# Optimization experiments

Hardware: AMD Instinct MI355X
Metric: run time of the kernel (lower is better)

## Reference

```python
import jax, jax.numpy as jnp
import numpy as np

# Kernel codes matching style 'L;O2;P2;Y2,1,1;R0.5;W1,1'
KERNEL_CODES = ['L', 'O', 'P', 'Y', 'R', 'W']
SM_TEMP = 1.0


def _norm_sq(q, k):
    # q: [n,l,h,e], k: [n,s,h,e] -> [n,h,l,s]
    q2 = jnp.einsum('nlhe,nlhe->nhl', q, q)[..., None]        # [n,h,l,1]
    k2 = jnp.einsum('nshe,nshe->nhs', k, k)[:, :, None, :]     # [n,h,1,s]
    qk = jnp.einsum('nlhe,nshe->nhls', q, k)
    return q2 + k2 - 2.0 * qk


def _kernel(code, q, k):
    if code == 'L':
        return jnp.einsum('nlhe,nshe->nhls', q, k)
    if code == 'O':  # -log(1 + ns^(p/2)), p=2
        return -jnp.log1p(_norm_sq(q, k))
    if code == 'P':  # -(ns)^(p/2), p=2
        return -_norm_sq(q, k)
    if code == 'Y':  # (alpha*<q,k> + c)^p, p=2, alpha=1, c=1
        d = jnp.einsum('nlhe,nshe->nhls', q, k)
        return (d + 1.0) ** 2
    if code == 'R':  # exp(-gamma*ns), gamma=0.5
        return jnp.exp(-0.5 * _norm_sq(q, k))
    if code == 'W':  # cos(ns/a)*exp(-ns/b), a=b=1
        ns = _norm_sq(q, k)
        return jnp.cos(ns) * jnp.exp(-ns)
    raise ValueError(code)


def setup_inputs() -> dict:
    key = jax.random.key(0)
    k1, k2, k3, k4 = jax.random.split(key, 4)
    N, L, S, H, E, K = 2, 1024, 1024, 8, 64, 6
    return {
        'query': jax.random.normal(k1, (N, L, H, E), dtype=jnp.float32),
        'key': jax.random.normal(k2, (N, S, H, E), dtype=jnp.float32),
        'attn_mask_add': jnp.zeros((N, L, S), dtype=jnp.float32),
        'key_lengths_add': jnp.zeros((N, S), dtype=jnp.float32),
        'M': jax.random.uniform(k3, (H, E, K), dtype=jnp.float32),
        'C': jax.random.uniform(k4, (K, H, E, E), dtype=jnp.float32),
    }


def reference(query, key, attn_mask_add, key_lengths_add, M, C):
    # mixture weights pi: [n,l,h,k]
    pi = jax.nn.softmax(jnp.einsum('nlhe,hek->nlhk', query, M), axis=-1)
    out = None
    for c, code in enumerate(KERNEL_CODES):
        # htilde = tanh(query @ C[c]): [n,l,h,e]
        htilde = jnp.tanh(jnp.einsum('nlhe,hef->nlhf', query, C[c]))
        qk = _kernel(code, htilde, key)                    # [n,h,l,s]
        qk = qk + attn_mask_add[:, None] + key_lengths_add[:, None, None, :]
        sm = jax.nn.softmax(SM_TEMP * qk, axis=-1)
        w = jnp.transpose(pi[..., c], (0, 2, 1))[..., None]  # [n,h,l,1]
        term = sm * w
        out = term if out is None else out + term
    return out
```

## Files before the change

### kernel.cpp

```cpp
#include <hip/hip_runtime.h>
#include <hip/hip_bf16.h>
#include <math.h>

#define N_  2
#define H_  8
#define G_  16
#define L_  1024
#define S_  1024
#define E_  64
#define NC_ 6

typedef __attribute__((ext_vector_type(4))) float floatx4;
typedef __attribute__((ext_vector_type(8))) short short8;

#define MFMA16 __builtin_amdgcn_mfma_f32_16x16x32_bf16

#define AHAT_OFF   0
#define AHAT_BYTES (NC_*G_*L_*128*2)
#define KHAT_OFF   (AHAT_OFF + AHAT_BYTES)
#define KHAT_BYTES (G_*S_*128*2)
#define PI_OFF     (KHAT_OFF + KHAT_BYTES)
#define PI_BYTES   (NC_*G_*L_*4)
#define HSQ_OFF    (PI_OFF + PI_BYTES)
#define HSQ_BYTES  (NC_*G_*L_*4)
#define KSQ_OFF    (HSQ_OFF + HSQ_BYTES)
#define KSQ_BYTES  (G_*S_*4)

__device__ __forceinline__ float ftanh(float x) {
  return 1.0f - 2.0f * __builtin_amdgcn_rcpf(__expf(2.0f*x) + 1.0f);
}

__global__ __launch_bounds__(256) void k_htilde(
    const float* __restrict__ q, const float* __restrict__ C,
    __hip_bfloat16* __restrict__ Ahat, float* __restrict__ hsq) {
  extern __shared__ char smraw[];
  float* qs = (float*)smraw;
  float* Cs = qs + 128*68;

  const int lch = blockIdx.x, c = blockIdx.y, g = blockIdx.z;
  const int n = g >> 3, h = g & 7;
  const int l0 = lch * 128;
  const int t = threadIdx.x;

  for (int u = t; u < 2048; u += 256) {
    int row = u >> 4, seg = u & 15;
    *(float4*)(qs + row*68 + seg*4) =
      *(const float4*)(q + (((size_t)(n*L_ + l0 + row))*H_ + h)*E_ + seg*4);
  }
  for (int u = t; u < 1024; u += 256) {
    int e = u >> 4, seg = u & 15;
    *(float4*)(Cs + e*68 + seg*4) =
      *(const float4*)(C + (((size_t)(c*8 + h))*64 + e)*64 + seg*4);
  }
  __syncthreads();

  const int rg = t >> 3, fg = t & 7;
  float acc[4][8];
  #pragma unroll
  for (int i = 0; i < 4; i++)
    #pragma unroll
    for (int j = 0; j < 8; j++) acc[i][j] = 0.0f;

  #pragma unroll 4
  for (int e0 = 0; e0 < 64; e0 += 4) {
    float4 q4[4];
    #pragma unroll
    for (int i = 0; i < 4; i++)
      q4[i] = *(const float4*)(qs + (rg*4 + i)*68 + e0);
    #pragma unroll
    for (int ee = 0; ee < 4; ee++) {
      float4 ca = *(const float4*)(Cs + (e0+ee)*68 + fg*8);
      float4 cb = *(const float4*)(Cs + (e0+ee)*68 + fg*8 + 4);
      float c8[8] = {ca.x, ca.y, ca.z, ca.w, cb.x, cb.y, cb.z, cb.w};
      #pragma unroll
      for (int i = 0; i < 4; i++) {
        float qv = (ee == 0) ? q4[i].x : (ee == 1) ? q4[i].y
                 : (ee == 2) ? q4[i].z : q4[i].w;
        #pragma unroll
        for (int j = 0; j < 8; j++) acc[i][j] = fmaf(qv, c8[j], acc[i][j]);
      }
    }
  }

  #pragma unroll
  for (int i = 0; i < 4; i++) {
    int l = l0 + rg*4 + i;
    size_t rowb = (((size_t)(c*G_ + g))*L_ + l) * 128;
    float ss = 0.0f;
    short8 hi8, lo8;
    #pragma unroll
    for (int j = 0; j < 8; j++) {
      float hv = ftanh(acc[i][j]);
      ss += hv*hv;
      __hip_bfloat16 hi = __float2bfloat16(hv);
      __hip_bfloat16 lo = __float2bfloat16(hv - __bfloat162float(hi));
      short hs, ls;
      __builtin_memcpy(&hs, &hi, 2);
      __builtin_memcpy(&ls, &lo, 2);
      hi8[j] = hs; lo8[j] = ls;
    }
    *(short8*)((char*)Ahat + (rowb + fg*8)*2)      = hi8;
    *(short8*)((char*)Ahat + (rowb + 64 + fg*8)*2) = lo8;
    ss += __shfl_xor(ss, 1); ss += __shfl_xor(ss, 2); ss += __shfl_xor(ss, 4);
    if (fg == 0) hsq[((size_t)(c*G_ + g))*L_ + l] = ss;
  }
}

__global__ __launch_bounds__(256) void k_pi(
    const float* __restrict__ q, const float* __restrict__ M,
    float* __restrict__ pi_t) {
  __shared__ float Ms[384];
  const int g = blockIdx.x >> 2, lch = blockIdx.x & 3;
  const int n = g >> 3, h = g & 7;
  const int t = threadIdx.x;
  const int l = lch*256 + t;
  for (int u = t; u < 384; u += 256) Ms[u] = M[h*384 + u];
  __syncthreads();
  const float* qrow = q + (((size_t)(n*L_ + l))*H_ + h)*E_;
  float p[6] = {0.f, 0.f, 0.f, 0.f, 0.f, 0.f};
  #pragma unroll 8
  for (int e = 0; e < 64; e++) {
    float qv = qrow[e];
    #pragma unroll
    for (int k = 0; k < 6; k++) p[k] = fmaf(qv, Ms[e*6 + k], p[k]);
  }
  float mx = p[0];
  #pragma unroll
  for (int k = 1; k < 6; k++) mx = fmaxf(mx, p[k]);
  float den = 0.f;
  #pragma unroll
  for (int k = 0; k < 6; k++) den += __expf(p[k] - mx);
  float rden = __builtin_amdgcn_rcpf(den);
  #pragma unroll
  for (int k = 0; k < 6; k++)
    pi_t[((size_t)(k*G_ + g))*L_ + l] = __expf(p[k] - mx) * rden;
}

__global__ __launch_bounds__(256) void k_key(
    const float* __restrict__ key, __hip_bfloat16* __restrict__ Khat,
    float* __restrict__ ksq) {
  int t = threadIdx.x; int wv = t >> 6; int lane = t & 63;
  int r = blockIdx.x*4 + wv;
  int g = r >> 10; int s = r & 1023; int n = g >> 3; int h = g & 7;
  float v = key[(((size_t)(n*S_ + s))*H_ + h)*E_ + lane];
  __hip_bfloat16 hi = __float2bfloat16(v);
  __hip_bfloat16 lo = __float2bfloat16(v - __bfloat162float(hi));
  size_t base = ((size_t)g*S_ + s)*128;
  Khat[base + lane]      = hi;
  Khat[base + 64 + lane] = lo;
  float sq = v*v;
  #pragma unroll
  for (int off = 32; off; off >>= 1) sq += __shfl_xor(sq, off);
  if (lane == 0) ksq[(size_t)g*S_ + s] = sq;
}

#define LDS_A6LO  0
#define LDS_ZRED  13824
#define LDS_MRED  15360
#define LDS_CST   16896
#define LDS_TOTAL 17664

__global__ __launch_bounds__(256, 2) void k_main(
    const __hip_bfloat16* __restrict__ Ahat, const __hip_bfloat16* __restrict__ Khat,
    const float* __restrict__ hsq, const float* __restrict__ ksq,
    const float* __restrict__ mask, const float* __restrict__ klen,
    const float* __restrict__ pi_t, float* __restrict__ out) {
  extern __shared__ char smraw[];
  char*   A6     = smraw + LDS_A6LO;
  float*  zred   = (float*)(smraw + LDS_ZRED);
  float*  mred   = (float*)(smraw + LDS_MRED);
  float2* cst    = (float2*)(smraw + LDS_CST);

  const int l0 = blockIdx.x * 16; const int g = blockIdx.y; const int n = g >> 3;
  const int t = threadIdx.x; const int w = t >> 6; const int lane = t & 63;
  const int quad = lane >> 4; const int lc = lane & 15;

  #pragma unroll
  for (int rep = 0; rep < 3; rep++) {
    int u = t + rep*256; int row = u >> 3, seg = u & 7;
    int cc = row >> 4, lr = row & 15;
    *(int4*)(A6 + row*144 + seg*16) =
      *(const int4*)((const char*)Ahat +
          (((size_t)(cc*G_ + g))*L_ + l0 + lr)*256 + 128 + seg*16);
  }

  short8 ah[6][2];
  #pragma unroll
  for (int cc = 0; cc < 6; cc++) {
    const char* arow = (const char*)Ahat + (((size_t)(cc*G_ + g))*L_ + l0 + lc)*256;
    ah[cc][0] = *(const short8*)(arow + quad*16);
    ah[cc][1] = *(const short8*)(arow + 64 + quad*16);
  }

  float h1p = 1.0f  + hsq[((size_t)(1*G_ + g))*L_ + l0 + lc];
  float nh2 = 64.0f - hsq[((size_t)(2*G_ + g))*L_ + l0 + lc];
  float h4h = -0.5f * hsq[((size_t)(4*G_ + g))*L_ + l0 + lc];
  float nh5 = -hsq[((size_t)(5*G_ + g))*L_ + l0 + lc];

  __syncthreads();

  auto LOADK = [&](int st, short8 (&bf)[4]) {
    const char* base = (const char*)Khat +
        (((size_t)g)*S_ + st*64 + w*16 + lc)*256 + quad*16;
    #pragma unroll
    for (int kt = 0; kt < 4; kt++)
      bf[kt] = *(const short8*)(base + kt*64);
  };

  float Zc0 = 0.f, Zc1 = 0.f, Zc2 = 0.f, Zc3 = 0.f, zp = 0.f;
  float m3 = -INFINITY, z3 = 0.f;

  auto SWEEP1 = [&](int st, const short8 (&bf)[4]) {
    int sb = st*64 + w*16 + quad*4;
    float4 mk4 = *(const float4*)(mask + ((size_t)(n*L_ + l0 + lc))*S_ + sb);
    float4 kl4 = *(const float4*)(klen + (size_t)n*S_ + sb);
    float4 kq4 = *(const float4*)(ksq  + (size_t)g*S_ + sb);
    float kq[4] = {kq4.x, kq4.y, kq4.z, kq4.w};
    float mv[4], Ev[4];
    mv[0] = mk4.x + kl4.x; mv[1] = mk4.y + kl4.y;
    mv[2] = mk4.z + kl4.z; mv[3] = mk4.w + kl4.w;
    #pragma unroll
    for (int i = 0; i < 4; i++) Ev[i] = __expf(mv[i]);
    #pragma unroll
    for (int c = 0; c < 6; c++) {
      short8 al0 = *(const short8*)(A6 + (c*16 + lc)*144 + quad*16);
      short8 al1 = *(const short8*)(A6 + (c*16 + lc)*144 + 64 + quad*16);
      floatx4 a = {0.f, 0.f, 0.f, 0.f};
      a = MFMA16(bf[0], ah[c][0], a, 0,0,0);
      a = MFMA16(bf[1], ah[c][1], a, 0,0,0);
      a = MFMA16(bf[0], al0,      a, 0,0,0);
      a = MFMA16(bf[1], al1,      a, 0,0,0);
      a = MFMA16(bf[2], ah[c][0], a, 0,0,0);
      a = MFMA16(bf[3], ah[c][1], a, 0,0,0);
      #pragma unroll
      for (int i = 0; i < 4; i++) {
        float d = a[i];
        if (c == 0) {
          Zc0 = fmaf(Ev[i], __expf(d), Zc0);
        } else if (c == 1) {
          Zc1 = fmaf(Ev[i], __builtin_amdgcn_rcpf(fmaf(-2.f, d, h1p + kq[i])), Zc1);
        } else if (c == 2) {
          zp += __expf(fmaf(2.f, d, nh2 - kq[i] + mv[i]));
        } else if (c == 3) {
          float tt = d + 1.f;
          float x  = fmaf(tt, tt, mv[i]);
          float mn = fmaxf(m3, x);
          float e  = __expf(fminf(m3, x) - mn);
          z3 = (x > m3) ? fmaf(z3, e, 1.0f) : (z3 + e);
          m3 = mn;
        } else if (c == 4) {
          Zc2 = fmaf(Ev[i], __expf(__expf(d + fmaf(-0.5f, kq[i], h4h))), Zc2);
        } else {
          float a5 = fmaf(2.f, d, nh5 - kq[i]);
          Zc3 = fmaf(Ev[i], __expf(__cosf(a5) * __expf(a5)), Zc3);
        }
      }
    }
  };

  {
    short8 bA[4], bB[4];
    LOADK(0, bA);
    #pragma unroll 1
    for (int st = 0; st < 16; st += 2) {
      LOADK(st + 1, bB);
      SWEEP1(st, bA);
      LOADK((st + 2) & 15, bA);
      SWEEP1(st + 1, bB);
    }
  }

  #pragma unroll
  for (int off = 16; off < 64; off <<= 1) {
    Zc0 += __shfl_xor(Zc0, off); Zc1 += __shfl_xor(Zc1, off);
    Zc2 += __shfl_xor(Zc2, off); Zc3 += __shfl_xor(Zc3, off);
    zp  += __shfl_xor(zp,  off);
    float mo = __shfl_xor(m3, off);
    float zo = __shfl_xor(z3, off);
    float mn = fmaxf(m3, mo);
    float e  = __expf(fminf(m3, mo) - mn);
    z3 = (mo > m3) ? fmaf(z3, e, zo) : fmaf(zo, e, z3);
    m3 = mn;
  }
  if (lane < 16) {
    zred[w*96 + 0*16 + lc] = Zc0; mred[w*96 + 0*16 + lc] = 0.f;
    zred[w*96 + 1*16 + lc] = Zc1; mred[w*96 + 1*16 + lc] = 0.f;
    zred[w*96 + 2*16 + lc] = zp;  mred[w*96 + 2*16 + lc] = 0.f;
    zred[w*96 + 3*16 + lc] = z3;  mred[w*96 + 3*16 + lc] = m3;
    zred[w*96 + 4*16 + lc] = Zc2; mred[w*96 + 4*16 + lc] = 0.f;
    zred[w*96 + 5*16 + lc] = Zc3; mred[w*96 + 5*16 + lc] = 0.f;
  }
  __syncthreads();
  if (t < 96) {
    int c = t >> 4;
    float z = zred[t], m = mred[t];
    if (c == 3) {
      #pragma unroll
      for (int w2 = 1; w2 < 4; w2++) {
        float mo = mred[w2*96 + t], zo = zred[w2*96 + t];
        float mn = fmaxf(m, mo);
        float e  = __expf(fminf(m, mo) - mn);
        z = (mo > m) ? fmaf(z, e, zo) : fmaf(zo, e, z);
        m = mn;
      }
    } else {
      #pragma unroll
      for (int w2 = 1; w2 < 4; w2++) z += zred[w2*96 + t];
    }
    float piv = pi_t[((size_t)((t >> 4)*G_ + g))*L_ + l0 + (t & 15)];
    cst[t] = make_float2(piv / z, m);
  }
  __syncthreads();

  float ac0 = cst[0*16 + lc].x, ac1 = cst[1*16 + lc].x, ac2 = cst[2*16 + lc].x;
  float ac3 = cst[3*16 + lc].x, ac4 = cst[4*16 + lc].x, ac5 = cst[5*16 + lc].x;
  float m3f = cst[3*16 + lc].y;

  auto SWEEP2 = [&](int st, const short8 (&bf)[4]) {
    int sb = st*64 + w*16 + quad*4;
    float4 mk4 = *(const float4*)(mask + ((size_t)(n*L_ + l0 + lc))*S_ + sb);
    float4 kl4 = *(const float4*)(klen + (size_t)n*S_ + sb);
    float4 kq4 = *(const float4*)(ksq  + (size_t)g*S_ + sb);
    float kq[4] = {kq4.x, kq4.y, kq4.z, kq4.w};
    float mv[4], Ev[4];
    mv[0] = mk4.x + kl4.x; mv[1] = mk4.y + kl4.y;
    mv[2] = mk4.z + kl4.z; mv[3] = mk4.w + kl4.w;
    #pragma unroll
    for (int i = 0; i < 4; i++) Ev[i] = __expf(mv[i]);
    float Sacc[4] = {0.f, 0.f, 0.f, 0.f};
    float Gg[4]   = {0.f, 0.f, 0.f, 0.f};
    #pragma unroll
    for (int c = 0; c < 6; c++) {
      short8 al0 = *(const short8*)(A6 + (c*16 + lc)*144 + quad*16);
      short8 al1 = *(const short8*)(A6 + (c*16 + lc)*144 + 64 + quad*16);
      floatx4 a = {0.f, 0.f, 0.f, 0.f};
      a = MFMA16(bf[0], ah[c][0], a, 0,0,0);
      a = MFMA16(bf[1], ah[c][1], a, 0,0,0);
      a = MFMA16(bf[0], al0,      a, 0,0,0);
      a = MFMA16(bf[1], al1,      a, 0,0,0);
      a = MFMA16(bf[2], ah[c][0], a, 0,0,0);
      a = MFMA16(bf[3], ah[c][1], a, 0,0,0);
      #pragma unroll
      for (int i = 0; i < 4; i++) {
        float d = a[i];
        if (c == 0) {
          Sacc[i] = fmaf(ac0, __expf(d), Sacc[i]);
        } else if (c == 1) {
          Sacc[i] = fmaf(ac1, __builtin_amdgcn_rcpf(fmaf(-2.f, d, h1p + kq[i])), Sacc[i]);
        } else if (c == 2) {
          Gg[i] = fmaf(ac2, __expf(fmaf(2.f, d, nh2 - kq[i] + mv[i])), Gg[i]);
        } else if (c == 3) {
          float tt = d + 1.f;
          float x  = fmaf(tt, tt, mv[i]);
          Gg[i] = fmaf(ac3, __expf(x - m3f), Gg[i]);
        } else if (c == 4) {
          Sacc[i] = fmaf(ac4, __expf(__expf(d + fmaf(-0.5f, kq[i], h4h))), Sacc[i]);
        } else {
          float a5 = fmaf(2.f, d, nh5 - kq[i]);
          Sacc[i] = fmaf(ac5, __expf(__cosf(a5) * __expf(a5)), Sacc[i]);
        }
      }
    }
    float4 ov;
    ov.x = fmaf(Ev[0], Sacc[0], Gg[0]);
    ov.y = fmaf(Ev[1], Sacc[1], Gg[1]);
    ov.z = fmaf(Ev[2], Sacc[2], Gg[2]);
    ov.w = fmaf(Ev[3], Sacc[3], Gg[3]);
    *(float4*)(out + (((size_t)g)*L_ + l0 + lc)*S_ + sb) = ov;
  };

  {
    short8 bA[4], bB[4];
    LOADK(0, bA);
    #pragma unroll 1
    for (int st = 0; st < 16; st += 2) {
      LOADK(st + 1, bB);
      SWEEP2(st, bA);
      LOADK((st + 2) & 15, bA);
      SWEEP2(st + 1, bB);
    }
  }
}

extern "C" void kernel_launch(void* const* d_in, const int* in_sizes, int n_in,
                              void* d_out, int out_size, void* d_ws, size_t ws_size,
                              hipStream_t stream) {
  (void)in_sizes; (void)n_in; (void)out_size; (void)ws_size;
  const float* q    = (const float*)d_in[0];
  const float* key  = (const float*)d_in[1];
  const float* mask = (const float*)d_in[2];
  const float* klen = (const float*)d_in[3];
  const float* M    = (const float*)d_in[4];
  const float* C    = (const float*)d_in[5];
  char* ws = (char*)d_ws;
  __hip_bfloat16* Ahat = (__hip_bfloat16*)(ws + AHAT_OFF);
  __hip_bfloat16* Khat = (__hip_bfloat16*)(ws + KHAT_OFF);
  float* pi_t    = (float*)(ws + PI_OFF);
  float* hsq     = (float*)(ws + HSQ_OFF);
  float* ksq     = (float*)(ws + KSQ_OFF);
  float* out = (float*)d_out;

  k_htilde<<<dim3(8, 6, 16), 256, 52224, stream>>>(q, C, Ahat, hsq);
  k_key<<<4096, 256, 0, stream>>>(key, Khat, ksq);
  k_pi<<<64, 256, 0, stream>>>(q, M, pi_t);
  k_main<<<dim3(64, 16), 256, LDS_TOTAL, stream>>>(Ahat, Khat, hsq, ksq, mask, klen,
                                                   pi_t, out);
}
```

Measured before the change: 202.7 us.

## Merge prep kernels, precombine mask and key lengths, restructure main loop

The three preprocessing kernels become one launch that dispatches on block index, and a new branch writes the sum of mask and key-length bias into an extra workspace buffer. The main kernel reads that single buffer instead of two arrays. It moves the hi parts of A for components 4 and 5 into LDS to cut register use. Both sweeps now issue all six MFMA groups before the transcendental math, with single-buffered prefetch of K and mask/ksq, and the mask is folded into the exponent arguments. In exchange, the combined mask buffer costs an extra 8MB write and read pass per call, and the A rows for components 4 and 5 are now read from LDS.

```diff
diff --git a/kernel.cpp b/kernel.cpp
--- a/kernel.cpp
+++ b/kernel.cpp
@@ -25,151 +25,170 @@
 #define HSQ_BYTES  (NC_*G_*L_*4)
 #define KSQ_OFF    (HSQ_OFF + HSQ_BYTES)
 #define KSQ_BYTES  (G_*S_*4)
+#define MKL_OFF    (KSQ_OFF + KSQ_BYTES)
+#define MKL_BYTES  (N_*L_*S_*4)
 
 __device__ __forceinline__ float ftanh(float x) {
   return 1.0f - 2.0f * __builtin_amdgcn_rcpf(__expf(2.0f*x) + 1.0f);
 }
 
-__global__ __launch_bounds__(256) void k_htilde(
+__global__ __launch_bounds__(256) void k_prep(
     const float* __restrict__ q, const float* __restrict__ C,
-    __hip_bfloat16* __restrict__ Ahat, float* __restrict__ hsq) {
+    const float* __restrict__ key, const float* __restrict__ M,
+    const float* __restrict__ mask, const float* __restrict__ klen,
+    __hip_bfloat16* __restrict__ Ahat, float* __restrict__ hsq,
+    __hip_bfloat16* __restrict__ Khat, float* __restrict__ ksq,
+    float* __restrict__ pi_t, float* __restrict__ mkl) {
   extern __shared__ char smraw[];
-  float* qs = (float*)smraw;
-  float* Cs = qs + 128*68;
-
-  const int lch = blockIdx.x, c = blockIdx.y, g = blockIdx.z;
-  const int n = g >> 3, h = g & 7;
-  const int l0 = lch * 128;
+  const int bx = blockIdx.x;
   const int t = threadIdx.x;
 
-  for (int u = t; u < 2048; u += 256) {
-    int row = u >> 4, seg = u & 15;
-    *(float4*)(qs + row*68 + seg*4) =
-      *(const float4*)(q + (((size_t)(n*L_ + l0 + row))*H_ + h)*E_ + seg*4);
-  }
-  for (int u = t; u < 1024; u += 256) {
-    int e = u >> 4, seg = u & 15;
-    *(float4*)(Cs + e*68 + seg*4) =
-      *(const float4*)(C + (((size_t)(c*8 + h))*64 + e)*64 + seg*4);
-  }
-  __syncthreads();
-
-  const int rg = t >> 3, fg = t & 7;
-  float acc[4][8];
-  #pragma unroll
-  for (int i = 0; i < 4; i++)
-    #pragma unroll
-    for (int j = 0; j < 8; j++) acc[i][j] = 0.0f;
-
-  #pragma unroll 4
-  for (int e0 = 0; e0 < 64; e0 += 4) {
-    float4 q4[4];
+  if (bx < 768) {
+    float* qs = (float*)smraw;
+    float* Cs = qs + 128*68;
+    const int g = bx / 48, r6 = bx % 48, c = r6 >> 3, lch = r6 & 7;
+    const int n = g >> 3, h = g & 7;
+    const int l0 = lch * 128;
+
+    for (int u = t; u < 2048; u += 256) {
+      int row = u >> 4, seg = u & 15;
+      *(float4*)(qs + row*68 + seg*4) =
+        *(const float4*)(q + (((size_t)(n*L_ + l0 + row))*H_ + h)*E_ + seg*4);
+    }
+    for (int u = t; u < 1024; u += 256) {
+      int e = u >> 4, seg = u & 15;
+      *(float4*)(Cs + e*68 + seg*4) =
+        *(const float4*)(C + (((size_t)(c*8 + h))*64 + e)*64 + seg*4);
+    }
+    __syncthreads();
+
+    const int rg = t >> 3, fg = t & 7;
+    float acc[4][8];
     #pragma unroll
     for (int i = 0; i < 4; i++)
-      q4[i] = *(const float4*)(qs + (rg*4 + i)*68 + e0);
-    #pragma unroll
-    for (int ee = 0; ee < 4; ee++) {
-      float4 ca = *(const float4*)(Cs + (e0+ee)*68 + fg*8);
-      float4 cb = *(const float4*)(Cs + (e0+ee)*68 + fg*8 + 4);
-      float c8[8] = {ca.x, ca.y, ca.z, ca.w, cb.x, cb.y, cb.z, cb.w};
-      #pragma unroll
-      for (int i = 0; i < 4; i++) {
-        float qv = (ee == 0) ? q4[i].x : (ee == 1) ? q4[i].y
-                 : (ee == 2) ? q4[i].z : q4[i].w;
+      #pragma unroll
+      for (int j = 0; j < 8; j++) acc[i][j] = 0.0f;
+
+    #pragma unroll 4
+    for (int e0 = 0; e0 < 64; e0 += 4) {
+      float4 q4[4];
+      #pragma unroll
+      for (int i = 0; i < 4; i++)
+        q4[i] = *(const float4*)(qs + (rg*4 + i)*68 + e0);
+      #pragma unroll
+      for (int ee = 0; ee < 4; ee++) {
+        float4 ca = *(const float4*)(Cs + (e0+ee)*68 + fg*8);
+        float4 cb = *(const float4*)(Cs + (e0+ee)*68 + fg*8 + 4);
+        float c8[8] = {ca.x, ca.y, ca.z, ca.w, cb.x, cb.y, cb.z, cb.w};
         #pragma unroll
-        for (int j = 0; j < 8; j++) acc[i][j] = fmaf(qv, c8[j], acc[i][j]);
-      }
-    }
-  }
-
-  #pragma unroll
-  for (int i = 0; i < 4; i++) {
-    int l = l0 + rg*4 + i;
-    size_t rowb = (((size_t)(c*G_ + g))*L_ + l) * 128;
-    float ss = 0.0f;
-    short8 hi8, lo8;
-    #pragma unroll
-    for (int j = 0; j < 8; j++) {
-      float hv = ftanh(acc[i][j]);
-      ss += hv*hv;
-      __hip_bfloat16 hi = __float2bfloat16(hv);
-      __hip_bfloat16 lo = __float2bfloat16(hv - __bfloat162float(hi));
-      short hs, ls;
-      __builtin_memcpy(&hs, &hi, 2);
-      __builtin_memcpy(&ls, &lo, 2);
-      hi8[j] = hs; lo8[j] = ls;
-    }
-    *(short8*)((char*)Ahat + (rowb + fg*8)*2)      = hi8;
-    *(short8*)((char*)Ahat + (rowb + 64 + fg*8)*2) = lo8;
-    ss += __shfl_xor(ss, 1); ss += __shfl_xor(ss, 2); ss += __shfl_xor(ss, 4);
-    if (fg == 0) hsq[((size_t)(c*G_ + g))*L_ + l] = ss;
+        for (int i = 0; i < 4; i++) {
+          float qv = (ee == 0) ? q4[i].x : (ee == 1) ? q4[i].y
+                   : (ee == 2) ? q4[i].z : q4[i].w;
+          #pragma unroll
+          for (int j = 0; j < 8; j++) acc[i][j] = fmaf(qv, c8[j], acc[i][j]);
+        }
+      }
+    }
+
+    #pragma unroll
+    for (int i = 0; i < 4; i++) {
+      int l = l0 + rg*4 + i;
+      size_t rowb = (((size_t)(c*G_ + g))*L_ + l) * 128;
+      float ss = 0.0f;
+      short8 hi8, lo8;
+      #pragma unroll
+      for (int j = 0; j < 8; j++) {
+        float hv = ftanh(acc[i][j]);
+        ss += hv*hv;
+        __hip_bfloat16 hi = __float2bfloat16(hv);
+        __hip_bfloat16 lo = __float2bfloat16(hv - __bfloat162float(hi));
+        short hs, ls;
+        __builtin_memcpy(&hs, &hi, 2);
+        __builtin_memcpy(&ls, &lo, 2);
+        hi8[j] = hs; lo8[j] = ls;
+      }
+      *(short8*)((char*)Ahat + (rowb + fg*8)*2)      = hi8;
+      *(short8*)((char*)Ahat + (rowb + 64 + fg*8)*2) = lo8;
+      ss += __shfl_xor(ss, 1); ss += __shfl_xor(ss, 2); ss += __shfl_xor(ss, 4);
+      if (fg == 0) hsq[((size_t)(c*G_ + g))*L_ + l] = ss;
+    }
+  } else if (bx < 1024) {
+    const int kb = bx - 768;
+    const int wv = t >> 6, lane = t & 63;
+    #pragma unroll 1
+    for (int it = 0; it < 16; it++) {
+      int r = kb*64 + it*4 + wv;
+      int g = r >> 10, s = r & 1023, n = g >> 3, h = g & 7;
+      float v = key[(((size_t)(n*S_ + s))*H_ + h)*E_ + lane];
+      __hip_bfloat16 hi = __float2bfloat16(v);
+      __hip_bfloat16 lo = __float2bfloat16(v - __bfloat162float(hi));
+      size_t base = ((size_t)g*S_ + s)*128;
+      Khat[base + lane]      = hi;
+      Khat[base + 64 + lane] = lo;
+      float sq = v*v;
+      #pragma unroll
+      for (int off = 32; off; off >>= 1) sq += __shfl_xor(sq, off);
+      if (lane == 0) ksq[(size_t)g*S_ + s] = sq;
+    }
+  } else if (bx < 1088) {
+    float* Ms = (float*)smraw;
+    const int pb = bx - 1024;
+    const int g = pb >> 2, lch = pb & 3;
+    const int n = g >> 3, h = g & 7;
+    const int l = lch*256 + t;
+    for (int u = t; u < 384; u += 256) Ms[u] = M[h*384 + u];
+    __syncthreads();
+    const float* qrow = q + (((size_t)(n*L_ + l))*H_ + h)*E_;
+    float p[6] = {0.f, 0.f, 0.f, 0.f, 0.f, 0.f};
+    #pragma unroll 8
+    for (int e = 0; e < 64; e++) {
+      float qv = qrow[e];
+      #pragma unroll
+      for (int k = 0; k < 6; k++) p[k] = fmaf(qv, Ms[e*6 + k], p[k]);
+    }
+    float mx = p[0];
+    #pragma unroll
+    for (int k = 1; k < 6; k++) mx = fmaxf(mx, p[k]);
+    float den = 0.f;
+    #pragma unroll
+    for (int k = 0; k < 6; k++) den += __expf(p[k] - mx);
+    float rden = __builtin_amdgcn_rcpf(den);
+    #pragma unroll
+    for (int k = 0; k < 6; k++)
+      pi_t[((size_t)(k*G_ + g))*L_ + l] = __expf(p[k] - mx) * rden;
+  } else {
+    const int mb = bx - 1088;
+    const float4* m4 = (const float4*)mask;
+    const float4* k4 = (const float4*)klen;
+    float4* o4 = (float4*)mkl;
+    #pragma unroll 1
+    for (int u = mb*256 + t; u < N_*L_*S_/4; u += 128*256) {
+      int n  = u >> 18;
+      int s4 = u & 255;
+      float4 a = m4[u], b = k4[n*256 + s4];
+      o4[u] = make_float4(a.x+b.x, a.y+b.y, a.z+b.z, a.w+b.w);
+    }
   }
 }
 
-__global__ __launch_bounds__(256) void k_pi(
-    const float* __restrict__ q, const float* __restrict__ M,
-    float* __restrict__ pi_t) {
-  __shared__ float Ms[384];
-  const int g = blockIdx.x >> 2, lch = blockIdx.x & 3;
-  const int n = g >> 3, h = g & 7;
-  const int t = threadIdx.x;
-  const int l = lch*256 + t;
-  for (int u = t; u < 384; u += 256) Ms[u] = M[h*384 + u];
-  __syncthreads();
-  const float* qrow = q + (((size_t)(n*L_ + l))*H_ + h)*E_;
-  float p[6] = {0.f, 0.f, 0.f, 0.f, 0.f, 0.f};
-  #pragma unroll 8
-  for (int e = 0; e < 64; e++) {
-    float qv = qrow[e];
-    #pragma unroll
-    for (int k = 0; k < 6; k++) p[k] = fmaf(qv, Ms[e*6 + k], p[k]);
-  }
-  float mx = p[0];
-  #pragma unroll
-  for (int k = 1; k < 6; k++) mx = fmaxf(mx, p[k]);
-  float den = 0.f;
-  #pragma unroll
-  for (int k = 0; k < 6; k++) den += __expf(p[k] - mx);
-  float rden = __builtin_amdgcn_rcpf(den);
-  #pragma unroll
-  for (int k = 0; k < 6; k++)
-    pi_t[((size_t)(k*G_ + g))*L_ + l] = __expf(p[k] - mx) * rden;
-}
-
-__global__ __launch_bounds__(256) void k_key(
-    const float* __restrict__ key, __hip_bfloat16* __restrict__ Khat,
-    float* __restrict__ ksq) {
-  int t = threadIdx.x; int wv = t >> 6; int lane = t & 63;
-  int r = blockIdx.x*4 + wv;
-  int g = r >> 10; int s = r & 1023; int n = g >> 3; int h = g & 7;
-  float v = key[(((size_t)(n*S_ + s))*H_ + h)*E_ + lane];
-  __hip_bfloat16 hi = __float2bfloat16(v);
-  __hip_bfloat16 lo = __float2bfloat16(v - __bfloat162float(hi));
-  size_t base = ((size_t)g*S_ + s)*128;
-  Khat[base + lane]      = hi;
-  Khat[base + 64 + lane] = lo;
-  float sq = v*v;
-  #pragma unroll
-  for (int off = 32; off; off >>= 1) sq += __shfl_xor(sq, off);
-  if (lane == 0) ksq[(size_t)g*S_ + s] = sq;
-}
-
 #define LDS_A6LO  0
-#define LDS_ZRED  13824
-#define LDS_MRED  15360
-#define LDS_CST   16896
-#define LDS_TOTAL 17664
+#define LDS_A45HI 13824
+#define LDS_ZRED  18432
+#define LDS_MRED  19968
+#define LDS_CST   21504
+#define LDS_TOTAL 22272
 
 __global__ __launch_bounds__(256, 2) void k_main(
     const __hip_bfloat16* __restrict__ Ahat, const __hip_bfloat16* __restrict__ Khat,
     const float* __restrict__ hsq, const float* __restrict__ ksq,
-    const float* __restrict__ mask, const float* __restrict__ klen,
-    const float* __restrict__ pi_t, float* __restrict__ out) {
+    const float* __restrict__ mkl, const float* __restrict__ pi_t,
+    float* __restrict__ out) {
   extern __shared__ char smraw[];
-  char*   A6     = smraw + LDS_A6LO;
-  float*  zred   = (float*)(smraw + LDS_ZRED);
-  float*  mred   = (float*)(smraw + LDS_MRED);
-  float2* cst    = (float2*)(smraw + LDS_CST);
+  char*   A6   = smraw + LDS_A6LO;
+  char*   A45  = smraw + LDS_A45HI;
+  float*  zred = (float*)(smraw + LDS_ZRED);
+  float*  mred = (float*)(smraw + LDS_MRED);
+  float2* cst  = (float2*)(smraw + LDS_CST);
 
   const int l0 = blockIdx.x * 16; const int g = blockIdx.y; const int n = g >> 3;
   const int t = threadIdx.x; const int w = t >> 6; const int lane = t & 63;
@@ -183,10 +202,17 @@
       *(const int4*)((const char*)Ahat +
           (((size_t)(cc*G_ + g))*L_ + l0 + lr)*256 + 128 + seg*16);
   }
-
-  short8 ah[6][2];
+  {
+    int row = t >> 3, seg = t & 7;
+    int cc = 4 + (row >> 4), lr = row & 15;
+    *(int4*)(A45 + row*144 + seg*16) =
+      *(const int4*)((const char*)Ahat +
+          (((size_t)(cc*G_ + g))*L_ + l0 + lr)*256 + seg*16);
+  }
+
+  short8 ah[4][2];
   #pragma unroll
-  for (int cc = 0; cc < 6; cc++) {
+  for (int cc = 0; cc < 4; cc++) {
     const char* arow = (const char*)Ahat + (((size_t)(cc*G_ + g))*L_ + l0 + lc)*256;
     ah[cc][0] = *(const short8*)(arow + quad*16);
     ah[cc][1] = *(const short8*)(arow + 64 + quad*16);
@@ -206,67 +232,63 @@
     for (int kt = 0; kt < 4; kt++)
       bf[kt] = *(const short8*)(base + kt*64);
   };
-
-  float Zc0 = 0.f, Zc1 = 0.f, Zc2 = 0.f, Zc3 = 0.f, zp = 0.f;
-  float m3 = -INFINITY, z3 = 0.f;
-
-  auto SWEEP1 = [&](int st, const short8 (&bf)[4]) {
+  auto LOADS = [&](int st, float4& mk4, float4& kq4) {
     int sb = st*64 + w*16 + quad*4;
-    float4 mk4 = *(const float4*)(mask + ((size_t)(n*L_ + l0 + lc))*S_ + sb);
-    float4 kl4 = *(const float4*)(klen + (size_t)n*S_ + sb);
-    float4 kq4 = *(const float4*)(ksq  + (size_t)g*S_ + sb);
-    float kq[4] = {kq4.x, kq4.y, kq4.z, kq4.w};
-    float mv[4], Ev[4];
-    mv[0] = mk4.x + kl4.x; mv[1] = mk4.y + kl4.y;
-    mv[2] = mk4.z + kl4.z; mv[3] = mk4.w + kl4.w;
-    #pragma unroll
-    for (int i = 0; i < 4; i++) Ev[i] = __expf(mv[i]);
+    mk4 = *(const float4*)(mkl + ((size_t)(n*L_ + l0 + lc))*S_ + sb);
+    kq4 = *(const float4*)(ksq + (size_t)g*S_ + sb);
+  };
+  auto MFMAPH = [&](const short8 (&bf)[4], floatx4 (&acc)[6]) {
     #pragma unroll
     for (int c = 0; c < 6; c++) {
+      short8 h0, h1;
+      if (c < 4) { h0 = ah[c][0]; h1 = ah[c][1]; }
+      else {
+        h0 = *(const short8*)(A45 + ((c-4)*16 + lc)*144 + quad*16);
+        h1 = *(const short8*)(A45 + ((c-4)*16 + lc)*144 + 64 + quad*16);
+      }
       short8 al0 = *(const short8*)(A6 + (c*16 + lc)*144 + quad*16);
       short8 al1 = *(const short8*)(A6 + (c*16 + lc)*144 + 64 + quad*16);
       floatx4 a = {0.f, 0.f, 0.f, 0.f};
-      a = MFMA16(bf[0], ah[c][0], a, 0,0,0);
-      a = MFMA16(bf[1], ah[c][1], a, 0,0,0);
-      a = MFMA16(bf[0], al0,      a, 0,0,0);
-      a = MFMA16(bf[1], al1,      a, 0,0,0);
-      a = MFMA16(bf[2], ah[c][0], a, 0,0,0);
-      a = MFMA16(bf[3], ah[c][1], a, 0,0,0);
+      a = MFMA16(bf[0], h0,  a, 0,0,0);
+      a = MFMA16(bf[1], h1,  a, 0,0,0);
+      a = MFMA16(bf[0], al0, a, 0,0,0);
+      a = MFMA16(bf[1], al1, a, 0,0,0);
+      a = MFMA16(bf[2], h0,  a, 0,0,0);
+      a = MFMA16(bf[3], h1,  a, 0,0,0);
+      acc[c] = a;
+    }
+  };
+
+  float Zc0 = 0.f, Zc1 = 0.f, Zc2 = 0.f, Zc3 = 0.f, zp = 0.f;
+  float m3 = -INFINITY, z3 = 0.f;
+
+  {
+    short8 bf[4]; float4 mk4, kq4;
+    LOADK(0, bf); LOADS(0, mk4, kq4);
+    #pragma unroll 1
+    for (int st = 0; st < 16; st++) {
+      floatx4 acc[6];
+      MFMAPH(bf, acc);
+      LOADK((st + 1) & 15, bf);
+      float mvv[4] = {mk4.x, mk4.y, mk4.z, mk4.w};
+      float kq[4]  = {kq4.x, kq4.y, kq4.z, kq4.w};
       #pragma unroll
       for (int i = 0; i < 4; i++) {
-        float d = a[i];
-        if (c == 0) {
-          Zc0 = fmaf(Ev[i], __expf(d), Zc0);
-        } else if (c == 1) {
-          Zc1 = fmaf(Ev[i], __builtin_amdgcn_rcpf(fmaf(-2.f, d, h1p + kq[i])), Zc1);
-        } else if (c == 2) {
-          zp += __expf(fmaf(2.f, d, nh2 - kq[i] + mv[i]));
-        } else if (c == 3) {
-          float tt = d + 1.f;
-          float x  = fmaf(tt, tt, mv[i]);
-          float mn = fmaxf(m3, x);
-          float e  = __expf(fminf(m3, x) - mn);
-          z3 = (x > m3) ? fmaf(z3, e, 1.0f) : (z3 + e);
-          m3 = mn;
-        } else if (c == 4) {
-          Zc2 = fmaf(Ev[i], __expf(__expf(d + fmaf(-0.5f, kq[i], h4h))), Zc2);
-        } else {
-          float a5 = fmaf(2.f, d, nh5 - kq[i]);
-          Zc3 = fmaf(Ev[i], __expf(__cosf(a5) * __expf(a5)), Zc3);
-        }
-      }
-    }
-  };
-
-  {
-    short8 bA[4], bB[4];
-    LOADK(0, bA);
-    #pragma unroll 1
-    for (int st = 0; st < 16; st += 2) {
-      LOADK(st + 1, bB);
-      SWEEP1(st, bA);
-      LOADK((st + 2) & 15, bA);
-      SWEEP1(st + 1, bB);
+        float Ev = __expf(mvv[i]);
+        Zc0 += __expf(acc[0][i] + mvv[i]);
+        Zc1 = fmaf(Ev, __builtin_amdgcn_rcpf(fmaf(-2.f, acc[1][i], h1p + kq[i])), Zc1);
+        zp += __expf(fmaf(2.f, acc[2][i], nh2 - kq[i] + mvv[i]));
+        float tt = acc[3][i] + 1.f;
+        float x  = fmaf(tt, tt, mvv[i]);
+        float mn = fmaxf(m3, x);
+        float e  = __expf(fminf(m3, x) - mn);
+        z3 = (x > m3) ? fmaf(z3, e, 1.0f) : (z3 + e);
+        m3 = mn;
+        Zc2 += __expf(__expf(acc[4][i] + fmaf(-0.5f, kq[i], h4h)) + mvv[i]);
+        float a5 = fmaf(2.f, acc[5][i], nh5 - kq[i]);
+        Zc3 += __expf(fmaf(__cosf(a5), __expf(a5), mvv[i]));
+      }
+      LOADS((st + 1) & 15, mk4, kq4);
     }
   }
 
@@ -316,68 +338,35 @@
   float ac3 = cst[3*16 + lc].x, ac4 = cst[4*16 + lc].x, ac5 = cst[5*16 + lc].x;
   float m3f = cst[3*16 + lc].y;
 
-  auto SWEEP2 = [&](int st, const short8 (&bf)[4]) {
-    int sb = st*64 + w*16 + quad*4;
-    float4 mk4 = *(const float4*)(mask + ((size_t)(n*L_ + l0 + lc))*S_ + sb);
-    float4 kl4 = *(const float4*)(klen + (size_t)n*S_ + sb);
-    float4 kq4 = *(const float4*)(ksq  + (size_t)g*S_ + sb);
-    float kq[4] = {kq4.x, kq4.y, kq4.z, kq4.w};
-    float mv[4], Ev[4];
-    mv[0] = mk4.x + kl4.x; mv[1] = mk4.y + kl4.y;
-    mv[2] = mk4.z + kl4.z; mv[3] = mk4.w + kl4.w;
-    #pragma unroll
-    for (int i = 0; i < 4; i++) Ev[i] = __expf(mv[i]);
-    float Sacc[4] = {0.f, 0.f, 0.f, 0.f};
-    float Gg[4]   = {0.f, 0.f, 0.f, 0.f};
-    #pragma unroll
-    for (int c = 0; c < 6; c++) {
-      short8 al0 = *(const short8*)(A6 + (c*16 + lc)*144 + quad*16);
-      short8 al1 = *(const short8*)(A6 + (c*16 + lc)*144 + 64 + quad*16);
-      floatx4 a = {0.f, 0.f, 0.f, 0.f};
-      a = MFMA16(bf[0], ah[c][0], a, 0,0,0);
-      a = MFMA16(bf[1], ah[c][1], a, 0,0,0);
-      a = MFMA16(bf[0], al0,      a, 0,0,0);
-      a = MFMA16(bf[1], al1,      a, 0,0,0);
-      a = MFMA16(bf[2], ah[c][0], a, 0,0,0);
-      a = MFMA16(bf[3], ah[c][1], a, 0,0,0);
+  {
+    short8 bf[4]; float4 mk4, kq4;
+    LOADK(0, bf); LOADS(0, mk4, kq4);
+    #pragma unroll 1
+    for (int st = 0; st < 16; st++) {
+      floatx4 acc[6];
+      MFMAPH(bf, acc);
+      LOADK((st + 1) & 15, bf);
+      float mvv[4] = {mk4.x, mk4.y, mk4.z, mk4.w};
+      float kq[4]  = {kq4.x, kq4.y, kq4.z, kq4.w};
+      float4 ov;
+      float ovv[4];
       #pragma unroll
       for (int i = 0; i < 4; i++) {
-        float d = a[i];
-        if (c == 0) {
-          Sacc[i] = fmaf(ac0, __expf(d), Sacc[i]);
-        } else if (c == 1) {
-          Sacc[i] = fmaf(ac1, __builtin_amdgcn_rcpf(fmaf(-2.f, d, h1p + kq[i])), Sacc[i]);
-        } else if (c == 2) {
-          Gg[i] = fmaf(ac2, __expf(fmaf(2.f, d, nh2 - kq[i] + mv[i])), Gg[i]);
-        } else if (c == 3) {
-          float tt = d + 1.f;
-          float x  = fmaf(tt, tt, mv[i]);
-          Gg[i] = fmaf(ac3, __expf(x - m3f), Gg[i]);
-        } else if (c == 4) {
-          Sacc[i] = fmaf(ac4, __expf(__expf(d + fmaf(-0.5f, kq[i], h4h))), Sacc[i]);
-        } else {
-          float a5 = fmaf(2.f, d, nh5 - kq[i]);
-          Sacc[i] = fmaf(ac5, __expf(__cosf(a5) * __expf(a5)), Sacc[i]);
-        }
-      }
-    }
-    float4 ov;
-    ov.x = fmaf(Ev[0], Sacc[0], Gg[0]);
-    ov.y = fmaf(Ev[1], Sacc[1], Gg[1]);
-    ov.z = fmaf(Ev[2], Sacc[2], Gg[2]);
-    ov.w = fmaf(Ev[3], Sacc[3], Gg[3]);
-    *(float4*)(out + (((size_t)g)*L_ + l0 + lc)*S_ + sb) = ov;
-  };
-
-  {
-    short8 bA[4], bB[4];
-    LOADK(0, bA);
-    #pragma unroll 1
-    for (int st = 0; st < 16; st += 2) {
-      LOADK(st + 1, bB);
-      SWEEP2(st, bA);
-      LOADK((st + 2) & 15, bA);
-      SWEEP2(st + 1, bB);
+        float Ev = __expf(mvv[i]);
+        float Gg = ac0 * __expf(acc[0][i] + mvv[i]);
+        float So = ac1 * __builtin_amdgcn_rcpf(fmaf(-2.f, acc[1][i], h1p + kq[i]));
+        Gg = fmaf(ac2, __expf(fmaf(2.f, acc[2][i], nh2 - kq[i] + mvv[i])), Gg);
+        float tt = acc[3][i] + 1.f;
+        Gg = fmaf(ac3, __expf(fmaf(tt, tt, mvv[i]) - m3f), Gg);
+        Gg = fmaf(ac4, __expf(__expf(acc[4][i] + fmaf(-0.5f, kq[i], h4h)) + mvv[i]), Gg);
+        float a5 = fmaf(2.f, acc[5][i], nh5 - kq[i]);
+        Gg = fmaf(ac5, __expf(fmaf(__cosf(a5), __expf(a5), mvv[i])), Gg);
+        ovv[i] = fmaf(Ev, So, Gg);
+      }
+      ov.x = ovv[0]; ov.y = ovv[1]; ov.z = ovv[2]; ov.w = ovv[3];
+      int sb = st*64 + w*16 + quad*4;
+      *(float4*)(out + (((size_t)g)*L_ + l0 + lc)*S_ + sb) = ov;
+      LOADS((st + 1) & 15, mk4, kq4);
     }
   }
 }
@@ -398,11 +387,11 @@
   float* pi_t    = (float*)(ws + PI_OFF);
   float* hsq     = (float*)(ws + HSQ_OFF);
   float* ksq     = (float*)(ws + KSQ_OFF);
+  float* mkl     = (float*)(ws + MKL_OFF);
   float* out = (float*)d_out;
 
-  k_htilde<<<dim3(8, 6, 16), 256, 52224, stream>>>(q, C, Ahat, hsq);
-  k_key<<<4096, 256, 0, stream>>>(key, Khat, ksq);
-  k_pi<<<64, 256, 0, stream>>>(q, M, pi_t);
-  k_main<<<dim3(64, 16), 256, LDS_TOTAL, stream>>>(Ahat, Khat, hsq, ksq, mask, klen,
+  k_prep<<<1216, 256, 52224, stream>>>(q, C, key, M, mask, klen,
+                                       Ahat, hsq, Khat, ksq, pi_t, mkl);
+  k_main<<<dim3(64, 16), 256, LDS_TOTAL, stream>>>(Ahat, Khat, hsq, ksq, mkl,
                                                    pi_t, out);
 }
```

Measured after the change: 204.8 us. About the same (+1.1%).
